# Performance work log

Hardware: AMD Instinct MI355X
Metric: run time of the kernel (lower is better)

## Reference

```python
import jax, jax.numpy as jnp
import numpy as np

EPS = 1e-10


def setup_inputs() -> dict:
    key = jax.random.key(0)
    kS, kQ, kW, kL = jax.random.split(key, 4)
    B, C, K, Q, D = 64, 20, 5, 15, 2048
    support = jax.random.normal(kS, (B * C * K, D), dtype=jnp.float32)
    query = jax.random.normal(kQ, (B * C * Q, D), dtype=jnp.float32)
    # encoder = single Linear(in_dim=D, hidden=D)
    W = jax.random.normal(kW, (D, D), dtype=jnp.float32) / np.sqrt(D)
    b = jnp.zeros((D,), dtype=jnp.float32)
    # one-hot support labels: each class appears K times per episode
    labels = jax.random.randint(kL, (B, C * K), 0, C)
    support_label_one_hot = jax.nn.one_hot(labels, C, dtype=jnp.float32)
    return {
        "support": support,
        "query": query,
        "support_label_one_hot": support_label_one_hot,
        "W": W,
        "b": b,
        "C": C,
        "K": K,
        "Q": Q,
    }


def reference(support, query, support_label_one_hot, W, b, C, K, Q):
    H = W.shape[1]
    # encoder (linear) on flat batches
    s = (support @ W + b).reshape(-1, C * K, H)   # [B, C*K, H]
    q = (query @ W + b).reshape(-1, C * Q, H)     # [B, C*Q, H]
    # DistanceNetwork: cosine-like similarity, only support magnitude normalized
    inv_norm = jax.lax.rsqrt(jnp.clip(jnp.sum(s * s, axis=-1), EPS, None))  # [B, C*K]
    sim = jnp.einsum("bqh,bsh->bqs", q, s) * inv_norm[:, None, :]           # [B, C*Q, C*K]
    # AttentionClassify: softmax over support set, then weighted sum of one-hot labels
    att = jax.nn.softmax(sim, axis=-1)                                       # [B, C*Q, C*K]
    preds = jnp.einsum("bqs,bsc->bqc", att, support_label_one_hot)          # [B, C*Q, C]
    probs = preds.reshape(-1, C)                                             # [B*C*Q, C]
    pred = jnp.argmax(probs, axis=1)
    return probs, pred
```

## Files before the change

### kernel.cpp

```cpp
#include <hip/hip_runtime.h>
#include <hip/hip_bf16.h>
#include <math.h>

#define BATCH 64
#define NCLS  20
#define NS    100
#define NQ    300
#define DIM   2048
#define MS    (BATCH * NS)
#define MQ    (BATCH * NQ)
#define KSPL  4
#define PROW  320
#define PCOL  112

typedef __attribute__((ext_vector_type(8))) short frag_ab;
typedef __attribute__((ext_vector_type(4))) float frag_cd;

union FAB { frag_ab f; unsigned u[4]; };

__device__ __forceinline__ unsigned rne_hi(float x) {
  unsigned u = __float_as_uint(x);
  return (u + 0x7FFFu + ((u >> 16) & 1u)) & 0xFFFF0000u;
}

__device__ __forceinline__ void split2rn(float x, float y, unsigned& p1,
                                         unsigned& p2) {
  union { __hip_bfloat162 h; unsigned u; } c1, c2;
  c1.h = __float22bfloat162_rn(make_float2(x, y));
  p1 = c1.u;
  float rx = x - __uint_as_float(c1.u << 16);
  float ry = y - __uint_as_float(c1.u & 0xFFFF0000u);
  c2.h = __float22bfloat162_rn(make_float2(rx, ry));
  p2 = c2.u;
}

#define GLL16(g, l)                                                            \
  __builtin_amdgcn_global_load_lds(                                            \
      (const __attribute__((address_space(1))) void*)(g),                      \
      (__attribute__((address_space(3))) void*)(l), 16, 0, 0)

__global__ __launch_bounds__(256) void esplit2(const float* __restrict__ X,
                                               unsigned short* __restrict__ X1,
                                               unsigned short* __restrict__ X2,
                                               int n4) {
  int i = blockIdx.x * 256 + threadIdx.x;
  if (i >= n4) return;
  float4 v = ((const float4*)X)[i];
  float x[4] = {v.x, v.y, v.z, v.w};
  ushort4 o1, o2;
  unsigned short* d1 = (unsigned short*)&o1;
  unsigned short* d2 = (unsigned short*)&o2;
#pragma unroll
  for (int q = 0; q < 4; ++q) {
    unsigned u1 = rne_hi(x[q]);
    float r1 = x[q] - __uint_as_float(u1);
    unsigned u2 = rne_hi(r1);
    d1[q] = (unsigned short)(u1 >> 16);
    d2[q] = (unsigned short)(u2 >> 16);
  }
  ((ushort4*)X1)[i] = o1;
  ((ushort4*)X2)[i] = o2;
}

template <int NH>
__global__ __launch_bounds__(256, 2) void gemm_mfma3(
    const float* __restrict__ X, const unsigned short* __restrict__ W1,
    const unsigned short* __restrict__ W2, const float* __restrict__ bias,
    float* __restrict__ Y) {
  __shared__ __align__(16) float          As[4][2][128][4];
  __shared__ __align__(16) unsigned short B1[4][128 * NH][8];
  __shared__ __align__(16) unsigned short B2[4][128 * NH][8];

  const int tid = threadIdx.x;
  const int w = tid >> 6, lane = tid & 63;
  const int ml = lane & 15, kq = lane >> 4;
  const int wm = (w >> 1) * 64, wn = (w & 1) * 64;
  const int col0 = blockIdx.x * (128 * NH), row0 = blockIdx.y * 128;

  frag_cd acc[NH][4][4];
#pragma unroll
  for (int h = 0; h < NH; ++h)
#pragma unroll
    for (int i = 0; i < 4; ++i)
#pragma unroll
      for (int j = 0; j < 4; ++j)
#pragma unroll
        for (int r = 0; r < 4; ++r) acc[h][i][j][r] = 0.f;

  for (int k0 = 0; k0 < DIM; k0 += 32) {
#pragma unroll
    for (int h = 0; h < 2; ++h)
#pragma unroll
      for (int mh = 0; mh < 2; ++mh) {
        const float* g =
            X + (size_t)(row0 + mh * 64 + lane) * DIM + k0 + w * 8 + h * 4;
        GLL16(g, &As[w][h][mh * 64][0]);
      }
#pragma unroll
    for (int t = 0; t < 2 * NH; ++t) {
      const size_t off = (size_t)(col0 + t * 64 + lane) * DIM + k0 + w * 8;
      GLL16(W1 + off, &B1[w][t * 64][0]);
      GLL16(W2 + off, &B2[w][t * 64][0]);
    }
    __syncthreads();

    FAB a1[4], a2[4];
#pragma unroll
    for (int i = 0; i < 4; ++i) {
      int m = wm + i * 16 + ml;
      float4 f0 = *(const float4*)&As[kq][0][m][0];
      float4 f1 = *(const float4*)&As[kq][1][m][0];
      split2rn(f0.x, f0.y, a1[i].u[0], a2[i].u[0]);
      split2rn(f0.z, f0.w, a1[i].u[1], a2[i].u[1]);
      split2rn(f1.x, f1.y, a1[i].u[2], a2[i].u[2]);
      split2rn(f1.z, f1.w, a1[i].u[3], a2[i].u[3]);
    }
#pragma unroll
    for (int nh = 0; nh < NH; ++nh) {
#pragma unroll
      for (int j = 0; j < 4; ++j) {
        int n = nh * 128 + wn + j * 16 + ml;
        FAB b1, b2;
        *(uint4*)&b1.u[0] = *(const uint4*)&B1[kq][n][0];
        *(uint4*)&b2.u[0] = *(const uint4*)&B2[kq][n][0];
#pragma unroll
        for (int i = 0; i < 4; ++i) {
          acc[nh][i][j] = __builtin_amdgcn_mfma_f32_16x16x32_bf16(
              a1[i].f, b1.f, acc[nh][i][j], 0, 0, 0);
          acc[nh][i][j] = __builtin_amdgcn_mfma_f32_16x16x32_bf16(
              a1[i].f, b2.f, acc[nh][i][j], 0, 0, 0);
          acc[nh][i][j] = __builtin_amdgcn_mfma_f32_16x16x32_bf16(
              a2[i].f, b1.f, acc[nh][i][j], 0, 0, 0);
        }
      }
    }
    __syncthreads();
  }

#pragma unroll
  for (int nh = 0; nh < NH; ++nh)
#pragma unroll
    for (int j = 0; j < 4; ++j) {
      int col = col0 + nh * 128 + wn + j * 16 + ml;
      float bv = bias ? bias[col] : 0.f;
#pragma unroll
      for (int i = 0; i < 4; ++i) {
        int rowb = row0 + wm + i * 16 + kq * 4;
#pragma unroll
        for (int r = 0; r < 4; ++r)
          Y[(size_t)(rowb + r) * DIM + col] = acc[nh][i][j][r] + bv;
      }
    }
}

#define MFMA3(ACC, A1, A2, BV1, BV2)                                           \
  ACC = __builtin_amdgcn_mfma_f32_16x16x32_bf16(A1.f, BV1.f, ACC, 0, 0, 0);    \
  ACC = __builtin_amdgcn_mfma_f32_16x16x32_bf16(A1.f, BV2.f, ACC, 0, 0, 0);    \
  ACC = __builtin_amdgcn_mfma_f32_16x16x32_bf16(A2.f, BV1.f, ACC, 0, 0, 0)

#define SIMJ(J)                                                                \
  {                                                                            \
    FAB bf1, bf2;                                                              \
    *(uint4*)&bf1.u[0] = *(const uint4*)(z1b + o##J + k0);                     \
    *(uint4*)&bf2.u[0] = *(const uint4*)(z2b + o##J + k0);                     \
    MFMA3(acc##J, a1, a2, bf1, bf2);                                           \
  }

#define STJ(J)                                                                 \
  {                                                                            \
    const int n = J * 16 + ml;                                                 \
    part[pbase + 0 * PCOL + n] = acc##J[0];                                    \
    part[pbase + 1 * PCOL + n] = acc##J[1];                                    \
    part[pbase + 2 * PCOL + n] = acc##J[2];                                    \
    part[pbase + 3 * PCOL + n] = acc##J[3];                                    \
  }

__global__ __launch_bounds__(256) void sim2_part(
    const float* __restrict__ Xq, const unsigned short* __restrict__ Z1,
    const unsigned short* __restrict__ Z2, float* __restrict__ part) {
  const int wg = blockIdx.x + 5 * blockIdx.y + 320 * blockIdx.z;
  const int swz = (wg & 7) * 160 + (wg >> 3);
  const int b = swz / 20;
  const int r20 = swz % 20;
  const int ks = r20 / 5;
  const int mt = r20 % 5;

  const int w = threadIdx.x >> 6, lane = threadIdx.x & 63;
  const int ml = lane & 15, kq = lane >> 4;

  int r = mt * 64 + w * 16 + ml;
  const int rc = r < NQ ? r : NQ - 1;
  const float* aptr = Xq + ((size_t)b * NQ + rc) * DIM + kq * 8;

  const unsigned short* z1b = Z1 + (size_t)b * NS * DIM + kq * 8;
  const unsigned short* z2b = Z2 + (size_t)b * NS * DIM + kq * 8;
  const int o0 = (0 * 16 + ml) * DIM;
  const int o1 = (1 * 16 + ml) * DIM;
  const int o2 = (2 * 16 + ml) * DIM;
  const int o3 = (3 * 16 + ml) * DIM;
  const int o4 = (4 * 16 + ml) * DIM;
  const int o5 = (5 * 16 + ml) * DIM;
  const int n6 = 6 * 16 + ml;
  const int o6 = (n6 < NS ? n6 : NS - 1) * DIM;

  frag_cd acc0 = {0.f, 0.f, 0.f, 0.f}, acc1 = {0.f, 0.f, 0.f, 0.f};
  frag_cd acc2 = {0.f, 0.f, 0.f, 0.f}, acc3 = {0.f, 0.f, 0.f, 0.f};
  frag_cd acc4 = {0.f, 0.f, 0.f, 0.f}, acc5 = {0.f, 0.f, 0.f, 0.f};
  frag_cd acc6 = {0.f, 0.f, 0.f, 0.f};

  const int kbeg = ks * (DIM / KSPL), kend = kbeg + DIM / KSPL;
#pragma unroll 2
  for (int k0 = kbeg; k0 < kend; k0 += 32) {
    float4 f0 = *(const float4*)(aptr + k0);
    float4 f1 = *(const float4*)(aptr + k0 + 4);
    FAB a1, a2;
    split2rn(f0.x, f0.y, a1.u[0], a2.u[0]);
    split2rn(f0.z, f0.w, a1.u[1], a2.u[1]);
    split2rn(f1.x, f1.y, a1.u[2], a2.u[2]);
    split2rn(f1.z, f1.w, a1.u[3], a2.u[3]);
    SIMJ(0); SIMJ(1); SIMJ(2); SIMJ(3); SIMJ(4); SIMJ(5); SIMJ(6);
  }

  const size_t pbase =
      (((size_t)ks * BATCH + b) * PROW + (mt * 64 + w * 16 + kq * 4)) * PCOL;
  STJ(0); STJ(1); STJ(2); STJ(3); STJ(4); STJ(5); STJ(6);
}

__global__ __launch_bounds__(256) void gemv_wb(const float* __restrict__ W,
                                               const float* __restrict__ b,
                                               float* __restrict__ wb,
                                               float* __restrict__ bb) {
  const int k = blockIdx.x;
  const int d0 = threadIdx.x * 8;
  float4 w0 = *(const float4*)(W + (size_t)k * DIM + d0);
  float4 w1 = *(const float4*)(W + (size_t)k * DIM + d0 + 4);
  float4 b0 = *(const float4*)(b + d0);
  float4 b1 = *(const float4*)(b + d0 + 4);
  float s = w0.x * b0.x + w0.y * b0.y + w0.z * b0.z + w0.w * b0.w +
            w1.x * b1.x + w1.y * b1.y + w1.z * b1.z + w1.w * b1.w;
#pragma unroll
  for (int off = 32; off; off >>= 1) s += __shfl_down(s, off, 64);
  __shared__ float red[4];
  if ((threadIdx.x & 63) == 0) red[threadIdx.x >> 6] = s;
  __syncthreads();
  if (threadIdx.x == 0) wb[k] = red[0] + red[1] + red[2] + red[3];
  if (k == 0) {
    float s2 = b0.x * b0.x + b0.y * b0.y + b0.z * b0.z + b0.w * b0.w +
               b1.x * b1.x + b1.y * b1.y + b1.z * b1.z + b1.w * b1.w;
#pragma unroll
    for (int off = 32; off; off >>= 1) s2 += __shfl_down(s2, off, 64);
    __syncthreads();
    if ((threadIdx.x & 63) == 0) red[threadIdx.x >> 6] = s2;
    __syncthreads();
    if (threadIdx.x == 0) bb[0] = red[0] + red[1] + red[2] + red[3];
  }
}

__global__ __launch_bounds__(256) void norm_v(const float* __restrict__ Z,
                                              const float* __restrict__ Xs,
                                              const float* __restrict__ wb,
                                              const float* __restrict__ bb,
                                              float* __restrict__ inv_norm,
                                              float* __restrict__ vv) {
  const int row = blockIdx.x;
  const int d0 = threadIdx.x * 8;
  const float* zp = Z + (size_t)row * DIM + d0;
  const float* xp = Xs + (size_t)row * DIM + d0;
  float4 z0 = *(const float4*)zp, z1 = *(const float4*)(zp + 4);
  float4 x0 = *(const float4*)xp, x1 = *(const float4*)(xp + 4);
  float4 w0 = *(const float4*)(wb + d0), w1 = *(const float4*)(wb + d0 + 4);
  float s1 = z0.x * x0.x + z0.y * x0.y + z0.z * x0.z + z0.w * x0.w +
             z1.x * x1.x + z1.y * x1.y + z1.z * x1.z + z1.w * x1.w;
  float s2 = x0.x * w0.x + x0.y * w0.y + x0.z * w0.z + x0.w * w0.w +
             x1.x * w1.x + x1.y * w1.y + x1.z * w1.z + x1.w * w1.w;
#pragma unroll
  for (int off = 32; off; off >>= 1) {
    s1 += __shfl_down(s1, off, 64);
    s2 += __shfl_down(s2, off, 64);
  }
  __shared__ float r1[4], r2[4];
  if ((threadIdx.x & 63) == 0) {
    r1[threadIdx.x >> 6] = s1;
    r2[threadIdx.x >> 6] = s2;
  }
  __syncthreads();
  if (threadIdx.x == 0) {
    float t1 = r1[0] + r1[1] + r1[2] + r1[3];
    float t2 = r2[0] + r2[1] + r2[2] + r2[3];
    float nn = t1 + 2.f * t2 + bb[0];
    inv_norm[row] = rsqrtf(fmaxf(nn, 1e-10f));
    vv[row] = t2;
  }
}

__global__ __launch_bounds__(256) void rowdot(const float* __restrict__ X,
                                              const float* __restrict__ wb,
                                              float* __restrict__ u) {
  const int row = blockIdx.x;
  const int d0 = threadIdx.x * 8;
  const float* xp = X + (size_t)row * DIM + d0;
  float4 x0 = *(const float4*)xp, x1 = *(const float4*)(xp + 4);
  float4 w0 = *(const float4*)(wb + d0), w1 = *(const float4*)(wb + d0 + 4);
  float s = x0.x * w0.x + x0.y * w0.y + x0.z * w0.z + x0.w * w0.w +
            x1.x * w1.x + x1.y * w1.y + x1.z * w1.z + x1.w * w1.w;
#pragma unroll
  for (int off = 32; off; off >>= 1) s += __shfl_down(s, off, 64);
  __shared__ float red[4];
  if ((threadIdx.x & 63) == 0) red[threadIdx.x >> 6] = s;
  __syncthreads();
  if (threadIdx.x == 0) u[row] = red[0] + red[1] + red[2] + red[3];
}

__global__ __launch_bounds__(256) void softmax_part(
    const float* __restrict__ part, const float* __restrict__ u,
    const float* __restrict__ vv, const float* __restrict__ bb,
    const float* __restrict__ inv_norm, const float* __restrict__ onehot,
    float* __restrict__ out) {
  const int wave = threadIdx.x >> 6;
  const int lane = threadIdx.x & 63;
  const int r = blockIdx.x * 4 + wave;
  const int b = r / NQ;
  const int m = r - b * NQ;
  const size_t kstr = (size_t)BATCH * PROW * PCOL;
  const float* p0 = part + ((size_t)b * PROW + m) * PCOL;
  const float bbv = bb[0];
  const float ur = u[r];

  float raw1 = p0[lane] + p0[kstr + lane] + p0[2 * kstr + lane] +
               p0[3 * kstr + lane];
  float v1 = (raw1 + ur + vv[b * NS + lane] + bbv) * inv_norm[b * NS + lane];
  float v2 = -INFINITY;
  if (lane < NS - 64) {
    const int n = lane + 64;
    float raw2 = p0[n] + p0[kstr + n] + p0[2 * kstr + n] + p0[3 * kstr + n];
    v2 = (raw2 + ur + vv[b * NS + n] + bbv) * inv_norm[b * NS + n];
  }
  float mx = fmaxf(v1, v2);
#pragma unroll
  for (int off = 32; off; off >>= 1) mx = fmaxf(mx, __shfl_xor(mx, off, 64));
  float e1 = expf(v1 - mx);
  float e2 = (lane < NS - 64) ? expf(v2 - mx) : 0.f;
  float ssum = e1 + e2;
#pragma unroll
  for (int off = 32; off; off >>= 1) ssum += __shfl_xor(ssum, off, 64);
  float inv = 1.0f / ssum;
  __shared__ float att[4][NS];
  __shared__ float pr[4][NCLS];
  att[wave][lane] = e1 * inv;
  if (lane < NS - 64) att[wave][lane + 64] = e2 * inv;
  __syncthreads();
  if (lane < NCLS) {
    const float* oh = onehot + ((size_t)b * NS) * NCLS + lane;
    float p = 0.f;
#pragma unroll 4
    for (int j = 0; j < NS; ++j) p += att[wave][j] * oh[(size_t)j * NCLS];
    out[(size_t)r * NCLS + lane] = p;
    pr[wave][lane] = p;
  }
  __syncthreads();
  if (lane == 0) {
    int best = 0;
    float bv = pr[wave][0];
    for (int c = 1; c < NCLS; ++c) {
      float v = pr[wave][c];
      if (v > bv) { bv = v; best = c; }
    }
    out[(size_t)MQ * NCLS + r] = (float)best;
  }
}

__global__ __launch_bounds__(256) void softmax_fb(
    const float* __restrict__ sim, const float* __restrict__ onehot,
    float* __restrict__ out) {
  const int wave = threadIdx.x >> 6;
  const int lane = threadIdx.x & 63;
  const int r = blockIdx.x * 4 + wave;
  const int b = r / NQ;
  const float* srow = sim + (size_t)r * NS;
  float v1 = srow[lane];
  float v2 = (lane < NS - 64) ? srow[lane + 64] : -INFINITY;
  float m = fmaxf(v1, v2);
#pragma unroll
  for (int off = 32; off; off >>= 1) m = fmaxf(m, __shfl_xor(m, off, 64));
  float e1 = expf(v1 - m);
  float e2 = (lane < NS - 64) ? expf(v2 - m) : 0.f;
  float ssum = e1 + e2;
#pragma unroll
  for (int off = 32; off; off >>= 1) ssum += __shfl_xor(ssum, off, 64);
  float inv = 1.0f / ssum;
  __shared__ float att[4][NS];
  __shared__ float pr[4][NCLS];
  att[wave][lane] = e1 * inv;
  if (lane < NS - 64) att[wave][lane + 64] = e2 * inv;
  __syncthreads();
  if (lane < NCLS) {
    const float* oh = onehot + ((size_t)b * NS) * NCLS + lane;
    float p = 0.f;
#pragma unroll 4
    for (int j = 0; j < NS; ++j) p += att[wave][j] * oh[(size_t)j * NCLS];
    out[(size_t)r * NCLS + lane] = p;
    pr[wave][lane] = p;
  }
  __syncthreads();
  if (lane == 0) {
    int best = 0;
    float bv = pr[wave][0];
    for (int c = 1; c < NCLS; ++c) {
      float v = pr[wave][c];
      if (v > bv) { bv = v; best = c; }
    }
    out[(size_t)MQ * NCLS + r] = (float)best;
  }
}

__global__ __launch_bounds__(256) void gemm_xw(const float* __restrict__ X,
                                               const float* __restrict__ W,
                                               const float* __restrict__ bias,
                                               float* __restrict__ Y) {
  __shared__ float As[16][64];
  __shared__ float Bs[16][64];
  const int t = threadIdx.x;
  const int row0 = blockIdx.x * 64;
  const int col0 = blockIdx.y * 64;
  const int am = t >> 2, ak = (t & 3) * 4;
  const int bk = t >> 4, bn = (t & 15) * 4;
  const int tm = (t >> 4) * 4, tn = (t & 15) * 4;
  float acc[4][4] = {};
  for (int k0 = 0; k0 < DIM; k0 += 16) {
    float4 av = *(const float4*)(X + (size_t)(row0 + am) * DIM + k0 + ak);
    As[ak + 0][am] = av.x;
    As[ak + 1][am] = av.y;
    As[ak + 2][am] = av.z;
    As[ak + 3][am] = av.w;
    *(float4*)&Bs[bk][bn] =
        *(const float4*)(W + (size_t)(k0 + bk) * DIM + col0 + bn);
    __syncthreads();
#pragma unroll
    for (int k = 0; k < 16; ++k) {
      float4 a4 = *(const float4*)&As[k][tm];
      float4 b4 = *(const float4*)&Bs[k][tn];
      float av_[4] = {a4.x, a4.y, a4.z, a4.w};
      float bv_[4] = {b4.x, b4.y, b4.z, b4.w};
#pragma unroll
      for (int i = 0; i < 4; ++i)
#pragma unroll
        for (int j = 0; j < 4; ++j) acc[i][j] += av_[i] * bv_[j];
    }
    __syncthreads();
  }
  float4 bbv = *(const float4*)(bias + col0 + tn);
  float bv_[4] = {bbv.x, bbv.y, bbv.z, bbv.w};
#pragma unroll
  for (int i = 0; i < 4; ++i) {
    float4 o;
    o.x = acc[i][0] + bv_[0];
    o.y = acc[i][1] + bv_[1];
    o.z = acc[i][2] + bv_[2];
    o.w = acc[i][3] + bv_[3];
    *(float4*)(Y + (size_t)(row0 + tm + i) * DIM + col0 + tn) = o;
  }
}

__global__ __launch_bounds__(256) void norm_kernel(const float* __restrict__ s,
                                                   float* __restrict__ inv_norm) {
  const int row = blockIdx.x;
  const float* p = s + (size_t)row * DIM;
  const int d0 = threadIdx.x * 8;
  float4 a = *(const float4*)(p + d0);
  float4 b = *(const float4*)(p + d0 + 4);
  float sum = a.x * a.x + a.y * a.y + a.z * a.z + a.w * a.w +
              b.x * b.x + b.y * b.y + b.z * b.z + b.w * b.w;
#pragma unroll
  for (int off = 32; off; off >>= 1) sum += __shfl_down(sum, off, 64);
  __shared__ float red[4];
  if ((threadIdx.x & 63) == 0) red[threadIdx.x >> 6] = sum;
  __syncthreads();
  if (threadIdx.x == 0) {
    float tot = red[0] + red[1] + red[2] + red[3];
    inv_norm[row] = rsqrtf(fmaxf(tot, 1e-10f));
  }
}

__global__ __launch_bounds__(256) void sim_kernel(const float* __restrict__ q,
                                                  const float* __restrict__ s,
                                                  const float* __restrict__ inv_norm,
                                                  float* __restrict__ sim) {
  __shared__ float As[16][64];
  __shared__ float Bs[16][64];
  const int t = threadIdx.x;
  const int b = blockIdx.z;
  const int row0 = blockIdx.y * 64;
  const int col0 = blockIdx.x * 64;
  const float* qb = q + (size_t)b * NQ * DIM;
  const float* sb = s + (size_t)b * NS * DIM;
  const int am = t >> 2, ak = (t & 3) * 4;
  const int tm = (t >> 4) * 4, tn = (t & 15) * 4;
  float acc[4][4] = {};
  for (int k0 = 0; k0 < DIM; k0 += 16) {
    float4 av = make_float4(0.f, 0.f, 0.f, 0.f);
    if (row0 + am < NQ)
      av = *(const float4*)(qb + (size_t)(row0 + am) * DIM + k0 + ak);
    As[ak + 0][am] = av.x;
    As[ak + 1][am] = av.y;
    As[ak + 2][am] = av.z;
    As[ak + 3][am] = av.w;
    float4 bv = make_float4(0.f, 0.f, 0.f, 0.f);
    if (col0 + am < NS)
      bv = *(const float4*)(sb + (size_t)(col0 + am) * DIM + k0 + ak);
    Bs[ak + 0][am] = bv.x;
    Bs[ak + 1][am] = bv.y;
    Bs[ak + 2][am] = bv.z;
    Bs[ak + 3][am] = bv.w;
    __syncthreads();
#pragma unroll
    for (int k = 0; k < 16; ++k) {
      float4 a4 = *(const float4*)&As[k][tm];
      float4 b4 = *(const float4*)&Bs[k][tn];
      float av_[4] = {a4.x, a4.y, a4.z, a4.w};
      float bv_[4] = {b4.x, b4.y, b4.z, b4.w};
#pragma unroll
      for (int i = 0; i < 4; ++i)
#pragma unroll
        for (int j = 0; j < 4; ++j) acc[i][j] += av_[i] * bv_[j];
    }
    __syncthreads();
  }
#pragma unroll
  for (int i = 0; i < 4; ++i) {
    int m = row0 + tm + i;
    if (m >= NQ) continue;
#pragma unroll
    for (int j = 0; j < 4; ++j) {
      int n = col0 + tn + j;
      if (n >= NS) continue;
      sim[((size_t)b * NQ + m) * NS + n] = acc[i][j] * inv_norm[b * NS + n];
    }
  }
}

extern "C" void kernel_launch(void* const* d_in, const int* in_sizes, int n_in,
                              void* d_out, int out_size, void* d_ws,
                              size_t ws_size, hipStream_t stream) {
  const float* support = (const float*)d_in[0];
  const float* query   = (const float*)d_in[1];
  const float* onehot  = (const float*)d_in[2];
  const float* W       = (const float*)d_in[3];
  const float* bias    = (const float*)d_in[4];

  char* wsb = (char*)d_ws;

  const size_t NEED = 163005444;

  if (ws_size >= NEED) {
    float* Z              = (float*)wsb;
    float* G              = (float*)(wsb + (size_t)52428800);
    unsigned short* Wr1   = (unsigned short*)(wsb + (size_t)69206016);
    unsigned short* Wr2   = (unsigned short*)(wsb + (size_t)77594624);
    unsigned short* G1    = (unsigned short*)(wsb + (size_t)85983232);
    unsigned short* G2    = (unsigned short*)(wsb + (size_t)94371840);
    unsigned short* Z1    = (unsigned short*)(wsb + (size_t)102760448);
    unsigned short* Z2    = (unsigned short*)(wsb + (size_t)128974848);
    float* part           = (float*)(wsb + (size_t)52428800);
    float* inv_norm       = (float*)(wsb + (size_t)162869248);
    float* vv             = (float*)(wsb + (size_t)162894848);
    float* u              = (float*)(wsb + (size_t)162920448);
    float* wb             = (float*)(wsb + (size_t)162997248);
    float* bb             = (float*)(wsb + (size_t)163005440);

    esplit2<<<DIM * DIM / 1024, 256, 0, stream>>>(W, Wr1, Wr2, DIM * DIM / 4);
    gemm_mfma3<1><<<dim3(DIM / 128, DIM / 128), 256, 0, stream>>>(
        W, Wr1, Wr2, nullptr, G);
    esplit2<<<DIM * DIM / 1024, 256, 0, stream>>>(G, G1, G2, DIM * DIM / 4);
    gemm_mfma3<2><<<dim3(DIM / 256, MS / 128), 256, 0, stream>>>(
        support, G1, G2, nullptr, Z);
    esplit2<<<MS * DIM / 1024, 256, 0, stream>>>(Z, Z1, Z2, MS * DIM / 4);
    gemv_wb<<<DIM, 256, 0, stream>>>(W, bias, wb, bb);
    norm_v<<<MS, 256, 0, stream>>>(Z, support, wb, bb, inv_norm, vv);
    rowdot<<<MQ, 256, 0, stream>>>(query, wb, u);
    sim2_part<<<dim3(5, BATCH, KSPL), 256, 0, stream>>>(query, Z1, Z2, part);
    softmax_part<<<MQ / 4, 256, 0, stream>>>(part, u, vv, bb, inv_norm,
                                             onehot, (float*)d_out);
  } else {
    float* s = (float*)wsb;
    float* q = (float*)(wsb + (size_t)52428800);
    float* inv_norm = q + (size_t)MQ * DIM;
    float* sim      = inv_norm + MS;
    gemm_xw<<<dim3(MS / 64, DIM / 64), 256, 0, stream>>>(support, W, bias, s);
    gemm_xw<<<dim3(MQ / 64, DIM / 64), 256, 0, stream>>>(query, W, bias, q);
    norm_kernel<<<MS, 256, 0, stream>>>(s, inv_norm);
    sim_kernel<<<dim3(2, 5, BATCH), 256, 0, stream>>>(q, s, inv_norm, sim);
    softmax_fb<<<MQ / 4, 256, 0, stream>>>(sim, onehot, (float*)d_out);
  }
}
```

Measured before the change: 841.5 us.

## Fuse bf16 split into GEMM epilogues and fold query-bias dot into sim kernel

The GEMM epilogue now writes the hi/lo bf16 split directly, so the two standalone esplit2 passes over G and Z go away and the fp32 G buffer is no longer stored. The separate rowdot kernel is removed: the query·wb dot product is accumulated inside sim2_part from the already-loaded query values, and softmax reduces the partials. The support GEMM changes from NH=2 to NH=1 tiles with a min-waves-per-EU bound of 3, which may raise register pressure. The epilogue stores are scattered 16-bit writes, which may coalesce less well than the separate split kernel's vector stores.

```diff
diff --git a/kernel.cpp b/kernel.cpp
--- a/kernel.cpp
+++ b/kernel.cpp
@@ -62,11 +62,12 @@
   ((ushort4*)X2)[i] = o2;
 }
 
-template <int NH>
-__global__ __launch_bounds__(256, 2) void gemm_mfma3(
+template <int NH, int MINW, bool SPLIT>
+__global__ __launch_bounds__(256, MINW) void gemm_mfma3(
     const float* __restrict__ X, const unsigned short* __restrict__ W1,
     const unsigned short* __restrict__ W2, const float* __restrict__ bias,
-    float* __restrict__ Y) {
+    float* __restrict__ Y, unsigned short* __restrict__ S1,
+    unsigned short* __restrict__ S2) {
   __shared__ __align__(16) float          As[4][2][128][4];
   __shared__ __align__(16) unsigned short B1[4][128 * NH][8];
   __shared__ __align__(16) unsigned short B2[4][128 * NH][8];
@@ -147,8 +148,18 @@
       for (int i = 0; i < 4; ++i) {
         int rowb = row0 + wm + i * 16 + kq * 4;
 #pragma unroll
-        for (int r = 0; r < 4; ++r)
-          Y[(size_t)(rowb + r) * DIM + col] = acc[nh][i][j][r] + bv;
+        for (int r = 0; r < 4; ++r) {
+          float val = acc[nh][i][j][r] + bv;
+          size_t idx = (size_t)(rowb + r) * DIM + col;
+          if (Y) Y[idx] = val;
+          if (SPLIT) {
+            unsigned u1 = rne_hi(val);
+            float rr = val - __uint_as_float(u1);
+            unsigned u2 = rne_hi(rr);
+            S1[idx] = (unsigned short)(u1 >> 16);
+            S2[idx] = (unsigned short)(u2 >> 16);
+          }
+        }
       }
     }
 }
@@ -177,7 +188,8 @@
 
 __global__ __launch_bounds__(256) void sim2_part(
     const float* __restrict__ Xq, const unsigned short* __restrict__ Z1,
-    const unsigned short* __restrict__ Z2, float* __restrict__ part) {
+    const unsigned short* __restrict__ Z2, const float* __restrict__ wb,
+    float* __restrict__ part, float* __restrict__ upart) {
   const int wg = blockIdx.x + 5 * blockIdx.y + 320 * blockIdx.z;
   const int swz = (wg & 7) * 160 + (wg >> 3);
   const int b = swz / 20;
@@ -207,12 +219,17 @@
   frag_cd acc2 = {0.f, 0.f, 0.f, 0.f}, acc3 = {0.f, 0.f, 0.f, 0.f};
   frag_cd acc4 = {0.f, 0.f, 0.f, 0.f}, acc5 = {0.f, 0.f, 0.f, 0.f};
   frag_cd acc6 = {0.f, 0.f, 0.f, 0.f};
+  float up = 0.f;
 
   const int kbeg = ks * (DIM / KSPL), kend = kbeg + DIM / KSPL;
 #pragma unroll 2
   for (int k0 = kbeg; k0 < kend; k0 += 32) {
     float4 f0 = *(const float4*)(aptr + k0);
     float4 f1 = *(const float4*)(aptr + k0 + 4);
+    float4 wa = *(const float4*)(wb + k0 + kq * 8);
+    float4 wc = *(const float4*)(wb + k0 + kq * 8 + 4);
+    up += f0.x * wa.x + f0.y * wa.y + f0.z * wa.z + f0.w * wa.w +
+          f1.x * wc.x + f1.y * wc.y + f1.z * wc.z + f1.w * wc.w;
     FAB a1, a2;
     split2rn(f0.x, f0.y, a1.u[0], a2.u[0]);
     split2rn(f0.z, f0.w, a1.u[1], a2.u[1]);
@@ -220,6 +237,11 @@
     split2rn(f1.z, f1.w, a1.u[3], a2.u[3]);
     SIMJ(0); SIMJ(1); SIMJ(2); SIMJ(3); SIMJ(4); SIMJ(5); SIMJ(6);
   }
+
+  up += __shfl_xor(up, 16, 64);
+  up += __shfl_xor(up, 32, 64);
+  if (lane < 16)
+    upart[((size_t)ks * BATCH + b) * PROW + mt * 64 + w * 16 + ml] = up;
 
   const size_t pbase =
       (((size_t)ks * BATCH + b) * PROW + (mt * 64 + w * 16 + kq * 4)) * PCOL;
@@ -293,26 +315,8 @@
   }
 }
 
-__global__ __launch_bounds__(256) void rowdot(const float* __restrict__ X,
-                                              const float* __restrict__ wb,
-                                              float* __restrict__ u) {
-  const int row = blockIdx.x;
-  const int d0 = threadIdx.x * 8;
-  const float* xp = X + (size_t)row * DIM + d0;
-  float4 x0 = *(const float4*)xp, x1 = *(const float4*)(xp + 4);
-  float4 w0 = *(const float4*)(wb + d0), w1 = *(const float4*)(wb + d0 + 4);
-  float s = x0.x * w0.x + x0.y * w0.y + x0.z * w0.z + x0.w * w0.w +
-            x1.x * w1.x + x1.y * w1.y + x1.z * w1.z + x1.w * w1.w;
-#pragma unroll
-  for (int off = 32; off; off >>= 1) s += __shfl_down(s, off, 64);
-  __shared__ float red[4];
-  if ((threadIdx.x & 63) == 0) red[threadIdx.x >> 6] = s;
-  __syncthreads();
-  if (threadIdx.x == 0) u[row] = red[0] + red[1] + red[2] + red[3];
-}
-
 __global__ __launch_bounds__(256) void softmax_part(
-    const float* __restrict__ part, const float* __restrict__ u,
+    const float* __restrict__ part, const float* __restrict__ upart,
     const float* __restrict__ vv, const float* __restrict__ bb,
     const float* __restrict__ inv_norm, const float* __restrict__ onehot,
     float* __restrict__ out) {
@@ -322,9 +326,11 @@
   const int b = r / NQ;
   const int m = r - b * NQ;
   const size_t kstr = (size_t)BATCH * PROW * PCOL;
+  const size_t ustr = (size_t)BATCH * PROW;
   const float* p0 = part + ((size_t)b * PROW + m) * PCOL;
+  const float* up0 = upart + (size_t)b * PROW + m;
   const float bbv = bb[0];
-  const float ur = u[r];
+  const float ur = up0[0] + up0[ustr] + up0[2 * ustr] + up0[3 * ustr];
 
   float raw1 = p0[lane] + p0[kstr + lane] + p0[2 * kstr + lane] +
                p0[3 * kstr + lane];
@@ -549,11 +555,10 @@
 
   char* wsb = (char*)d_ws;
 
-  const size_t NEED = 163005444;
+  const size_t NEED = 163333376;
 
   if (ws_size >= NEED) {
     float* Z              = (float*)wsb;
-    float* G              = (float*)(wsb + (size_t)52428800);
     unsigned short* Wr1   = (unsigned short*)(wsb + (size_t)69206016);
     unsigned short* Wr2   = (unsigned short*)(wsb + (size_t)77594624);
     unsigned short* G1    = (unsigned short*)(wsb + (size_t)85983232);
@@ -563,22 +568,20 @@
     float* part           = (float*)(wsb + (size_t)52428800);
     float* inv_norm       = (float*)(wsb + (size_t)162869248);
     float* vv             = (float*)(wsb + (size_t)162894848);
-    float* u              = (float*)(wsb + (size_t)162920448);
     float* wb             = (float*)(wsb + (size_t)162997248);
     float* bb             = (float*)(wsb + (size_t)163005440);
+    float* upart          = (float*)(wsb + (size_t)163005696);
 
     esplit2<<<DIM * DIM / 1024, 256, 0, stream>>>(W, Wr1, Wr2, DIM * DIM / 4);
-    gemm_mfma3<1><<<dim3(DIM / 128, DIM / 128), 256, 0, stream>>>(
-        W, Wr1, Wr2, nullptr, G);
-    esplit2<<<DIM * DIM / 1024, 256, 0, stream>>>(G, G1, G2, DIM * DIM / 4);
-    gemm_mfma3<2><<<dim3(DIM / 256, MS / 128), 256, 0, stream>>>(
-        support, G1, G2, nullptr, Z);
-    esplit2<<<MS * DIM / 1024, 256, 0, stream>>>(Z, Z1, Z2, MS * DIM / 4);
+    gemm_mfma3<1, 3, true><<<dim3(DIM / 128, DIM / 128), 256, 0, stream>>>(
+        W, Wr1, Wr2, nullptr, nullptr, G1, G2);
+    gemm_mfma3<1, 3, true><<<dim3(DIM / 128, MS / 128), 256, 0, stream>>>(
+        support, G1, G2, nullptr, Z, Z1, Z2);
     gemv_wb<<<DIM, 256, 0, stream>>>(W, bias, wb, bb);
     norm_v<<<MS, 256, 0, stream>>>(Z, support, wb, bb, inv_norm, vv);
-    rowdot<<<MQ, 256, 0, stream>>>(query, wb, u);
-    sim2_part<<<dim3(5, BATCH, KSPL), 256, 0, stream>>>(query, Z1, Z2, part);
-    softmax_part<<<MQ / 4, 256, 0, stream>>>(part, u, vv, bb, inv_norm,
+    sim2_part<<<dim3(5, BATCH, KSPL), 256, 0, stream>>>(query, Z1, Z2, wb,
+                                                        part, upart);
+    softmax_part<<<MQ / 4, 256, 0, stream>>>(part, upart, vv, bb, inv_norm,
                                              onehot, (float*)d_out);
   } else {
     float* s = (float*)wsb;
```

Measured after the change: 902.9 us. 1.07x slower.
